# Kernel optimization log

Measured on AMD Instinct MI355X. Metric: run time of the kernel, lower is better.

## Reference

```python
import jax, jax.numpy as jnp
import numpy as np
from jax import lax

# dims: batch, time, in_channels, out_channels, numerator order, denominator order
B, T, I, O, NB, NA = 16, 4096, 32, 32, 3, 2


def setup_inputs() -> dict:
    key = jax.random.key(0)
    k1, k2, k3 = jax.random.split(key, 3)
    u_in = jax.random.normal(k1, (B, T, I), dtype=jnp.float32)
    # parameters initialized as in the module: randn * 0.1
    b_coeff = jax.random.normal(k2, (O, I, NB), dtype=jnp.float32) * 0.1
    a_coeff = jax.random.normal(k3, (O, I, NA), dtype=jnp.float32) * 0.1
    return {"u_in": u_in, "b_coeff": b_coeff, "a_coeff": a_coeff}


def _mimo_filter(u_in, b_coeff, a_coeff):
    """y[b,t,o] = sum_i IIR_{o,i}(u[b,:,i])[t], zero initial conditions.

    Per pair (o,i): y_oi[t] = sum_k b[o,i,k]*u[t-k,i] - sum_j a[o,i,j]*y_oi[t-j].
    """
    dtype = u_in.dtype
    n_b = b_coeff.shape[-1]
    n_a = a_coeff.shape[-1]
    t_len = u_in.shape[1]

    # FIR (numerator) part, vectorized: x[b,t,o,i] = sum_k b[o,i,k] * u[b,t-k,i]
    u_pad = jnp.pad(u_in, ((0, 0), (n_b - 1, 0), (0, 0)))
    # (B, T, I, n_b): lag-k slice of u for each tap k
    u_lags = jnp.stack([u_pad[:, n_b - 1 - k: n_b - 1 - k + t_len, :]
                        for k in range(n_b)], axis=-1)
    x = jnp.einsum('btik,oik->btoi', u_lags, b_coeff)  # (B, T, O, I)

    # IIR (denominator) recursion via scan over time.
    a = a_coeff  # (O, I, n_a)

    def step(y_hist, x_t):
        # y_hist: (B, O, I, n_a) most-recent-first; x_t: (B, O, I)
        y_t = x_t - jnp.einsum('boij,oij->boi', y_hist, a)
        y_hist = jnp.concatenate([y_t[..., None], y_hist[..., :-1]], axis=-1)
        return y_hist, y_t

    x_tfirst = jnp.moveaxis(x, 1, 0)  # (T, B, O, I)
    init = jnp.zeros(x.shape[:1] + x.shape[2:] + (n_a,), dtype=dtype)  # (B,O,I,n_a)
    _, y_pairs = lax.scan(step, init, x_tfirst)  # (T, B, O, I)
    # sum over input channels -> (B, T, O)
    return jnp.moveaxis(y_pairs, 0, 1).sum(axis=-1)


def reference(u_in, b_coeff, a_coeff):
    return _mimo_filter(u_in, b_coeff, a_coeff)
```

## Files before the change

kernel.cpp:

```cpp
#include <hip/hip_runtime.h>

constexpr int B = 16, T = 4096, I = 32, O = 32;
constexpr int C = 16, L = T / C, W = 64;
constexpr int TT = 32;
constexpr int NC = L / TT;
constexpr int ROWW = 36;

__global__ __launch_bounds__(256) void mimo_iir_kernel(
    const float* __restrict__ u,
    const float* __restrict__ bcf,
    const float* __restrict__ acf,
    float* __restrict__ out)
{
    __shared__ float tile[8][TT][ROWW];

    const int tid = threadIdx.x;
    const int i  = tid & 31;
    const int g  = tid >> 5;
    const int gg = blockIdx.x * 8 + g;
    const int o  = gg & (O - 1);
    const int bc = gg >> 5;
    const int c  = bc & (C - 1);
    const int b  = bc >> 4;

    const float* bw = bcf + (o * I + i) * 3;
    const float b0 = bw[0], b1 = bw[1], b2 = bw[2];
    const float* aw = acf + (o * I + i) * 2;
    const float a1 = aw[0], a2 = aw[1];

    const float* ub = u + ((size_t)b * T) * I + i;
    const int t0 = c * L;

    float y1 = 0.f, y2 = 0.f, u1, u2;
    float uv[TT];

    if (c != 0) {
        const float* wp = ub + (size_t)(t0 - W) * I;
        u1 = wp[-I];
        u2 = wp[-2 * I];
#pragma unroll
        for (int blk = 0; blk < W / TT; ++blk) {
#pragma unroll
            for (int k = 0; k < TT; ++k) uv[k] = wp[k * I];
#pragma unroll
            for (int k = 0; k < TT; ++k) {
                const float u0 = uv[k];
                const float x = fmaf(b0, u0, fmaf(b1, u1, b2 * u2));
                const float y = fmaf(-a1, y1, fmaf(-a2, y2, x));
                y2 = y1; y1 = y; u2 = u1; u1 = u0;
            }
            wp += TT * I;
        }
    } else {
        u1 = 0.f; u2 = 0.f;
    }

    const float* mp = ub + (size_t)t0 * I;
    float* op = out + ((size_t)b * T + t0) * O + o;
    const float4* row = reinterpret_cast<const float4*>(&tile[g][i][0]);

    for (int ch = 0; ch < NC; ++ch) {
#pragma unroll
        for (int k = 0; k < TT; ++k) uv[k] = mp[k * I];
#pragma unroll
        for (int k = 0; k < TT; ++k) {
            const float u0 = uv[k];
            const float x = fmaf(b0, u0, fmaf(b1, u1, b2 * u2));
            const float y = fmaf(-a1, y1, fmaf(-a2, y2, x));
            y2 = y1; y1 = y; u2 = u1; u1 = u0;
            tile[g][k][i] = y;
        }
        __builtin_amdgcn_sched_barrier(0);
        float4 s0 = row[0], s1 = row[1], s2 = row[2], s3 = row[3];
        s0 += row[4]; s1 += row[5]; s2 += row[6]; s3 += row[7];
        const float4 s = (s0 + s1) + (s2 + s3);
        op[(ch * TT + i) * (size_t)O] = (s.x + s.y) + (s.z + s.w);
        __builtin_amdgcn_sched_barrier(0);
        mp += TT * I;
    }
}

extern "C" void kernel_launch(void* const* d_in, const int* in_sizes, int n_in,
                              void* d_out, int out_size, void* d_ws, size_t ws_size,
                              hipStream_t stream) {
    const float* u   = (const float*)d_in[0];
    const float* bcf = (const float*)d_in[1];
    const float* acf = (const float*)d_in[2];
    float* out = (float*)d_out;

    const int total_threads = B * C * O * 32;
    const int block = 256;
    const int grid = total_threads / block;
    mimo_iir_kernel<<<grid, block, 0, stream>>>(u, bcf, acf, out);
}
```

Baseline: 77.96 us.

## Replace LDS tile reduction with cross-lane DPP/swizzle butterfly reduce; double chunks

Replaces the shared-memory transpose-and-sum over input channels with an in-register recursive-halving reduction using ds_swizzle and DPP row moves, so each lane ends up holding the sum for one time step. The time dimension is split into twice as many chunks with a shorter warm-up window, which increases parallelism and cuts redundant warm-up work. Launch bounds now request higher occupancy. The shorter warm-up window relies on the IIR decaying fast enough and may change accuracy slightly; the lane-permutation constants must be correct for 32-lane groups within a 64-wide wavefront.

```diff
diff --git a/kernel.cpp b/kernel.cpp
--- a/kernel.cpp
+++ b/kernel.cpp
@@ -1,19 +1,24 @@
 #include <hip/hip_runtime.h>
 
 constexpr int B = 16, T = 4096, I = 32, O = 32;
-constexpr int C = 16, L = T / C, W = 64;
-constexpr int TT = 32;
-constexpr int NC = L / TT;
-constexpr int ROWW = 36;
+constexpr int C = 32, L = T / C, W = 32;
+constexpr int TT = 32, NC = L / TT;
 
-__global__ __launch_bounds__(256) void mimo_iir_kernel(
+template <int CTRL>
+__device__ __forceinline__ float dppmov(float x) {
+    return __int_as_float(__builtin_amdgcn_update_dpp(
+        0, __float_as_int(x), CTRL, 0xF, 0xF, true));
+}
+__device__ __forceinline__ float swz16(float x) {
+    return __int_as_float(__builtin_amdgcn_ds_swizzle(__float_as_int(x), 0x401F));
+}
+
+__global__ __launch_bounds__(256, 8) void mimo_iir_kernel(
     const float* __restrict__ u,
     const float* __restrict__ bcf,
     const float* __restrict__ acf,
     float* __restrict__ out)
 {
-    __shared__ float tile[8][TT][ROWW];
-
     const int tid = threadIdx.x;
     const int i  = tid & 31;
     const int g  = tid >> 5;
@@ -21,61 +26,82 @@
     const int o  = gg & (O - 1);
     const int bc = gg >> 5;
     const int c  = bc & (C - 1);
-    const int b  = bc >> 4;
+    const int b  = bc >> 5;
 
     const float* bw = bcf + (o * I + i) * 3;
     const float b0 = bw[0], b1 = bw[1], b2 = bw[2];
     const float* aw = acf + (o * I + i) * 2;
-    const float a1 = aw[0], a2 = aw[1];
+    const float na1 = -aw[0], na2 = -aw[1];
 
     const float* ub = u + ((size_t)b * T) * I + i;
     const int t0 = c * L;
 
-    float y1 = 0.f, y2 = 0.f, u1, u2;
-    float uv[TT];
+    float y1 = 0.f, y2 = 0.f, u1 = 0.f, u2 = 0.f;
+    float y[TT];
 
     if (c != 0) {
-        const float* wp = ub + (size_t)(t0 - W) * I;
-        u1 = wp[-I];
-        u2 = wp[-2 * I];
+        const int ts = t0 - W;
+        u1 = ub[(ts - 1) * I];
+        u2 = ub[(ts - 2) * I];
+        const float* wp = ub + (size_t)ts * I;
 #pragma unroll
-        for (int blk = 0; blk < W / TT; ++blk) {
+        for (int k = 0; k < TT; ++k) y[k] = wp[k * I];
 #pragma unroll
-            for (int k = 0; k < TT; ++k) uv[k] = wp[k * I];
-#pragma unroll
-            for (int k = 0; k < TT; ++k) {
-                const float u0 = uv[k];
-                const float x = fmaf(b0, u0, fmaf(b1, u1, b2 * u2));
-                const float y = fmaf(-a1, y1, fmaf(-a2, y2, x));
-                y2 = y1; y1 = y; u2 = u1; u1 = u0;
-            }
-            wp += TT * I;
+        for (int k = 0; k < TT; ++k) {
+            const float u0 = y[k];
+            const float x  = fmaf(b0, u0, fmaf(b1, u1, b2 * u2));
+            const float yy = fmaf(na1, y1, fmaf(na2, y2, x));
+            y2 = y1; y1 = yy; u2 = u1; u1 = u0;
         }
-    } else {
-        u1 = 0.f; u2 = 0.f;
     }
 
     const float* mp = ub + (size_t)t0 * I;
-    float* op = out + ((size_t)b * T + t0) * O + o;
-    const float4* row = reinterpret_cast<const float4*>(&tile[g][i][0]);
+    float* op = out + ((size_t)(b * T + t0) + i) * O + o;
+
+    const bool l4 = i & 16, l3 = i & 8, l2 = i & 4, l1 = i & 2, l0 = i & 1;
 
     for (int ch = 0; ch < NC; ++ch) {
 #pragma unroll
-        for (int k = 0; k < TT; ++k) uv[k] = mp[k * I];
+        for (int k = 0; k < TT; ++k) y[k] = mp[k * I];
 #pragma unroll
         for (int k = 0; k < TT; ++k) {
-            const float u0 = uv[k];
-            const float x = fmaf(b0, u0, fmaf(b1, u1, b2 * u2));
-            const float y = fmaf(-a1, y1, fmaf(-a2, y2, x));
-            y2 = y1; y1 = y; u2 = u1; u1 = u0;
-            tile[g][k][i] = y;
+            const float u0 = y[k];
+            const float x  = fmaf(b0, u0, fmaf(b1, u1, b2 * u2));
+            const float yy = fmaf(na1, y1, fmaf(na2, y2, x));
+            y2 = y1; y1 = yy; u2 = u1; u1 = u0;
+            y[k] = yy;
         }
-        __builtin_amdgcn_sched_barrier(0);
-        float4 s0 = row[0], s1 = row[1], s2 = row[2], s3 = row[3];
-        s0 += row[4]; s1 += row[5]; s2 += row[6]; s3 += row[7];
-        const float4 s = (s0 + s1) + (s2 + s3);
-        op[(ch * TT + i) * (size_t)O] = (s.x + s.y) + (s.z + s.w);
-        __builtin_amdgcn_sched_barrier(0);
+#pragma unroll
+        for (int m = 0; m < 16; ++m) {
+            const float keep = l4 ? y[m + 16] : y[m];
+            const float give = l4 ? y[m] : y[m + 16];
+            y[m] = keep + swz16(give);
+        }
+#pragma unroll
+        for (int m = 0; m < 8; ++m) {
+            const float keep = l3 ? y[m + 8] : y[m];
+            const float give = l3 ? y[m] : y[m + 8];
+            y[m] = keep + dppmov<0x140>(give);
+        }
+#pragma unroll
+        for (int m = 0; m < 4; ++m) {
+            const float keep = l2 ? y[m + 4] : y[m];
+            const float give = l2 ? y[m] : y[m + 4];
+            y[m] = keep + dppmov<0x141>(give);
+        }
+#pragma unroll
+        for (int m = 0; m < 2; ++m) {
+            const float keep = l1 ? y[m + 2] : y[m];
+            const float give = l1 ? y[m] : y[m + 2];
+            y[m] = keep + dppmov<0x4E>(give);
+        }
+        {
+            const float keep = l0 ? y[1] : y[0];
+            const float give = l0 ? y[0] : y[1];
+            y[0] = keep + dppmov<0xB1>(give);
+        }
+        *op = y[0];
+        op += (size_t)TT * O;
         mp += TT * I;
     }
 }
```

Measured after the change: 80.26 us. 1.03x slower.
